# Performance work log

Measured on AMD Instinct MI355X. Metric: run time of the kernel, lower is better.

The kernel has to match this reference:

```python
import jax, jax.numpy as jnp
import numpy as np
from jax import lax

EPS = 1e-6            # cfg.positive
GAUSS_DIM = (32, 32)  # cfg.iou_gauss_dim
TOP_K_CONF = 100      # cfg.nms_top_k_conf
TOP_K_IOU = 20        # cfg.nms_top_k_iou


def unnormal_gaussian(mask_shape, loc):
    # loc: [B, N, 4] = (cx, cy, w, h) in normalized [0,1] coords.
    # Unnormalized anisotropic gaussian rendered on an HxW grid.
    H, W = mask_shape
    cx, cy, w, h = loc[..., 0], loc[..., 1], loc[..., 2], loc[..., 3]
    ys = (jnp.arange(H, dtype=loc.dtype) + 0.5) / H
    xs = (jnp.arange(W, dtype=loc.dtype) + 0.5) / W
    dx = (xs[None, None, None, :] - cx[..., None, None]) / (w[..., None, None] + 1e-4)
    dy = (ys[None, None, :, None] - cy[..., None, None]) / (h[..., None, None] + 1e-4)
    return jnp.exp(-0.5 * (dx * dx + dy * dy))  # [B, N, H, W]


def _take2(t, idx):
    # twoIndexThree: t [B,N,D], idx [B,K] -> [B,K,D]
    return jnp.take_along_axis(t, idx[..., None], axis=1)


def detect(conf, loc, mask):
    # conf: [B,P] object scores; loc: [B,P,4]; mask: [B,P,Dm]
    sorted_conf, idx = lax.top_k(conf, TOP_K_CONF)
    sorted_loc = _take2(loc, idx)
    sorted_mask = _take2(mask, idx)
    g = unnormal_gaussian(GAUSS_DIM, sorted_loc)  # [B,N,Hg,Wg]
    # pairwise gaussian IoU: sum(min) / sum(max); use min+max == a+b identity
    inter = jnp.sum(jnp.minimum(g[:, :, None], g[:, None, :]), axis=(-2, -1))  # [B,N,N]
    s = jnp.sum(g, axis=(-2, -1))
    union = s[:, :, None] + s[:, None, :] - inter
    iou = inter / union
    iou_max = jnp.max(jnp.triu(iou, 1), axis=1)   # max overlap with any earlier (higher-conf) box
    _, keep = lax.top_k(-iou_max, TOP_K_IOU)      # keep K least-overlapping boxes
    return iou, sorted_loc, sorted_mask, sorted_conf, keep


def ae_scaled_loss(original, iou, keep, loc, conf):
    conf_matrix = conf[:, :, None] * conf[:, None, :]   # outer product [B,N,N]
    final_scale = iou * jnp.triu(conf_matrix, 1)
    kept_loc = _take2(loc, keep)                        # [B,K,4]
    # surrogate AutoEncoder per-box loss (AutoEncoder class not in source)
    ae_loss = jnp.mean(kept_loc ** 2, axis=-1)          # [B,K]
    B, N = final_scale.shape[0], final_scale.shape[1]
    K = keep.shape[1]
    ae_grid = jnp.zeros_like(final_scale).at[jnp.arange(B)[:, None], keep].set(
        jnp.broadcast_to(ae_loss[..., None], (B, K, N)))
    return jnp.mean(ae_grid * final_scale)


def variance_loss(original, loc, mask, conf, proto):
    B, C, H, W = original.shape
    Hp, Wp = proto.shape[1], proto.shape[2]
    ug = unnormal_gaussian((Hp, Wp), loc)                           # [B,K,Hp,Wp]
    assembled = jax.nn.sigmoid(jnp.einsum('bhwp,bkp->bkhw', proto, mask))  # lincomb
    attention = assembled * ug
    mc = attention * conf[:, :, None, None]                         # maskConfidence
    denom = jnp.sum(mc, axis=1, keepdims=True) + EPS
    final_conf = 1.0 - jnp.sum(mc * mc / denom, axis=1)             # [B,Hp,Wp]
    final_conf = jnp.where(jnp.isnan(final_conf), 0.0, final_conf)
    # bilinear, align_corners=False == jax linear resize (half-pixel centers)
    resized = jax.image.resize(final_conf[:, None], (B, 1, H, W), method='linear')[:, 0]
    total = jnp.sum(resized, axis=0)                                 # [H,W]
    wmean = jnp.einsum('bchw,bhw->chw', original, resized) / total
    sq = (original - wmean) ** 2
    wvar = sq * resized[:, None] / (total + EPS)
    return jnp.sum(wvar) / Hp * B


def reference(original, loc, conf, mask, proto):
    conf_p = jax.nn.softmax(conf, axis=2)[:, :, 1]
    iou, s_loc, s_mask, s_conf, keep = detect(conf_p, loc, mask)
    ae = ae_scaled_loss(original, iou, keep, s_loc, s_conf)
    k_loc = _take2(s_loc, keep)
    k_mask = _take2(s_mask, keep)
    k_conf = jnp.take_along_axis(s_conf, keep, axis=1)
    var = variance_loss(original, k_loc, k_mask, k_conf, proto)
    return jnp.stack([var, ae])  # [variance_loss, ae_loss]


def setup_inputs() -> dict:
    key = jax.random.key(0)
    k1, k2, k3, k4, k5, k6 = jax.random.split(key, 6)
    B, P, Dm = 2, 19248, 32
    H = W = 550
    Hp = Wp = 138
    original = jax.random.normal(k1, (B, 3, H, W), dtype=jnp.float32)
    centers = jax.random.uniform(k2, (B, P, 2), dtype=jnp.float32)
    sizes = jax.random.uniform(k3, (B, P, 2), dtype=jnp.float32, minval=0.1, maxval=0.5)
    loc = jnp.concatenate([centers, sizes], axis=-1)                 # (cx,cy,w,h)
    conf = jax.random.normal(k4, (B, P, 2), dtype=jnp.float32)
    mask = jax.random.normal(k5, (B, P, Dm), dtype=jnp.float32) * 0.2
    proto = jax.random.normal(k6, (B, Hp, Wp, Dm), dtype=jnp.float32) * 0.5
    return {"original": original, "loc": loc, "conf": conf, "mask": mask, "proto": proto}
```

## Files before the change

kernel.cpp:

```cpp
#include <hip/hip_runtime.h>
#include <hip/hip_bf16.h>
#include <math.h>

constexpr int B   = 2;
constexpr int P   = 19248;
constexpr int N   = 100;
constexpr int K   = 20;
constexpr int GD  = 32;
constexpr int GP  = GD * GD;
constexpr int HP  = 138;
constexpr int HPP = HP * HP;
constexpr int H   = 550;
constexpr int W   = 550;
constexpr int DM  = 32;
constexpr float EPS = 1e-6f;
constexpr int NBIN = 2048;
constexpr int CAND_MAX = 4096;
constexpr int NPAIR = N * (N - 1) / 2;

constexpr int OFS_IDX   = 0;
constexpr int OFS_SCONF = OFS_IDX   + B * N;
constexpr int OFS_SLOC  = OFS_SCONF + B * N;
constexpr int OFS_G     = OFS_SLOC  + B * N * 4;
constexpr int OFS_S     = OFS_G     + B * N * GP;
constexpr int OFS_IOU   = OFS_S     + B * N;
constexpr int OFS_KLOC  = OFS_IOU   + B * N * N;
constexpr int OFS_KMASK = OFS_KLOC  + B * K * 4;
constexpr int OFS_KCONF = OFS_KMASK + B * K * DM;
constexpr int OFS_FC    = OFS_KCONF + B * K;
constexpr int OFS_HIST  = OFS_FC    + B * HPP;
constexpr int OFS_CCNT  = OFS_HIST  + B * NBIN;
constexpr int OFS_T     = OFS_CCNT  + B;
constexpr int OFS_CVAL  = OFS_T     + B;
constexpr int OFS_CIDX  = OFS_CVAL  + B * CAND_MAX;

__device__ __forceinline__ float sig_conf(const float* __restrict__ conf, int b, int p) {
  float c0 = conf[(b * P + p) * 2 + 0];
  float c1 = conf[(b * P + p) * 2 + 1];
  float m  = fmaxf(c0, c1);
  float e0 = expf(c0 - m), e1 = expf(c1 - m);
  return e1 / (e0 + e1);
}

__global__ __launch_bounds__(256) void k_hist(const float* __restrict__ conf,
                                              int* __restrict__ wsi,
                                              float* __restrict__ out) {
  const int b = blockIdx.y, t = threadIdx.x;
  if (blockIdx.x == 0 && b == 0 && t < 2) out[t] = 0.0f;
  __shared__ int sh[NBIN];
  for (int q = t; q < NBIN; q += 256) sh[q] = 0;
  __syncthreads();
  const int base = blockIdx.x * 1024;
#pragma unroll
  for (int q = 0; q < 4; q++) {
    int p = base + q * 256 + t;
    if (p < P) {
      float v = sig_conf(conf, b, p);
      atomicAdd(&sh[__float_as_uint(v) >> 19], 1);
    }
  }
  __syncthreads();
  for (int q = t; q < NBIN; q += 256) {
    int c = sh[q];
    if (c) atomicAdd(&wsi[OFS_HIST + b * NBIN + q], c);
  }
}

__global__ __launch_bounds__(256) void k_thresh(int* __restrict__ wsi) {
  const int b = blockIdx.x, t = threadIdx.x;
  __shared__ int sh[NBIN];
  for (int q = t; q < NBIN; q += 256) sh[q] = wsi[OFS_HIST + b * NBIN + q];
  __syncthreads();
  if (t == 0) {
    int acc = 0, bin = NBIN - 1;
    for (; bin >= 0; bin--) { acc += sh[bin]; if (acc >= N) break; }
    wsi[OFS_T + b] = bin;
  }
}

__global__ __launch_bounds__(256) void k_compact(const float* __restrict__ conf,
                                                 float* __restrict__ wsf,
                                                 int* __restrict__ wsi) {
  const int b = blockIdx.y, t = threadIdx.x;
  const int T = wsi[OFS_T + b];
  const int base = blockIdx.x * 1024;
#pragma unroll
  for (int q = 0; q < 4; q++) {
    int p = base + q * 256 + t;
    if (p < P) {
      float v = sig_conf(conf, b, p);
      if ((int)(__float_as_uint(v) >> 19) >= T) {
        int pos = atomicAdd(&wsi[OFS_CCNT + b], 1);
        if (pos < CAND_MAX) {
          wsf[OFS_CVAL + b * CAND_MAX + pos] = v;
          wsi[OFS_CIDX + b * CAND_MAX + pos] = p;
        }
      }
    }
  }
}

__global__ __launch_bounds__(1024) void k_rank(const float* __restrict__ loc,
                                               float* __restrict__ wsf,
                                               int* __restrict__ wsi) {
  const int b = blockIdx.x, t = threadIdx.x;
  const int M = min(wsi[OFS_CCNT + b], CAND_MAX);
  constexpr int CPT = CAND_MAX / 1024;
  __shared__ float tv[1024];
  __shared__ int   ti[1024];
  __shared__ float outv[N];
  __shared__ int   outi[N];

  float mv[CPT]; int mi[CPT]; int rank[CPT];
#pragma unroll
  for (int q = 0; q < CPT; q++) {
    int c = t + q * 1024;
    rank[q] = 0;
    if (c < M) { mv[q] = wsf[OFS_CVAL + b * CAND_MAX + c]; mi[q] = wsi[OFS_CIDX + b * CAND_MAX + c]; }
    else       { mv[q] = -1.0f; mi[q] = -1; }
  }
  for (int tile = 0; tile < M; tile += 1024) {
    int len = min(1024, M - tile);
    __syncthreads();
    if (t < len) { tv[t] = wsf[OFS_CVAL + b * CAND_MAX + tile + t]; ti[t] = wsi[OFS_CIDX + b * CAND_MAX + tile + t]; }
    __syncthreads();
    for (int j = 0; j < len; j++) {
      float jv = tv[j]; int ji = ti[j];
#pragma unroll
      for (int q = 0; q < CPT; q++)
        rank[q] += (jv > mv[q] || (jv == mv[q] && ji < mi[q])) ? 1 : 0;
    }
  }
#pragma unroll
  for (int q = 0; q < CPT; q++) {
    int c = t + q * 1024;
    if (c < M && rank[q] < N) { outv[rank[q]] = mv[q]; outi[rank[q]] = mi[q]; }
  }
  __syncthreads();

  if (t < N) {
    wsi[OFS_IDX + b * N + t]   = outi[t];
    wsf[OFS_SCONF + b * N + t] = outv[t];
  }
  for (int q = t; q < N * 4; q += 1024) {
    int k = q >> 2, d = q & 3;
    wsf[OFS_SLOC + (b * N + k) * 4 + d] = loc[(b * P + outi[k]) * 4 + d];
  }
}

__global__ __launch_bounds__(256) void ul_gauss_kernel(float* __restrict__ wsf) {
  const int blk = blockIdx.x;
  const int t = threadIdx.x;
  const int i = blk % N;
  const float* l = &wsf[OFS_SLOC + blk * 4];
  const float cx = l[0], cy = l[1], bw = l[2], bh = l[3];
  float* g = &wsf[OFS_G + blk * GP];
  float lsum = 0.0f;
#pragma unroll
  for (int q = 0; q < 4; q++) {
    int pix = t + q * 256;
    int y = pix >> 5, x = pix & 31;
    float dx = ((x + 0.5f) / 32.0f - cx) / (bw + 1e-4f);
    float dy = ((y + 0.5f) / 32.0f - cy) / (bh + 1e-4f);
    float gv = expf(-0.5f * (dx * dx + dy * dy));
    g[pix] = gv;
    lsum += gv;
  }
  for (int q = t; q <= i; q += 256) wsf[OFS_IOU + blk * N + q] = 0.0f;
  for (int off = 32; off > 0; off >>= 1) lsum += __shfl_down(lsum, off);
  __shared__ float sp[4];
  if ((t & 63) == 0) sp[t >> 6] = lsum;
  __syncthreads();
  if (t == 0) wsf[OFS_S + blk] = sp[0] + sp[1] + sp[2] + sp[3];
}

__global__ __launch_bounds__(256) void ul_iou_kernel(float* __restrict__ wsf) {
  const int blk = blockIdx.x;
  const int b = blk / NPAIR;
  const int r = blk - b * NPAIR;
  int i = (int)((199.0f - sqrtf((float)(39601 - 8 * r))) * 0.5f);
  i = min(max(i, 0), N - 2);
  while (i < N - 2 && ((i + 1) * (2 * N - 2 - i)) / 2 <= r) i++;
  while (i > 0 && (i * (2 * N - 1 - i)) / 2 > r) i--;
  const int j = i + 1 + (r - (i * (2 * N - 1 - i)) / 2);

  const int t = threadIdx.x;
  const float* gi = &wsf[OFS_G + (b * N + i) * GP];
  const float* gj = &wsf[OFS_G + (b * N + j) * GP];
  float lsum = 0.0f;
#pragma unroll
  for (int q = 0; q < 4; q++) {
    int pix = t + q * 256;
    lsum += fminf(gi[pix], gj[pix]);
  }
  for (int off = 32; off > 0; off >>= 1) lsum += __shfl_down(lsum, off);
  __shared__ float sp[4];
  if ((t & 63) == 0) sp[t >> 6] = lsum;
  __syncthreads();
  if (t == 0) {
    float inter = sp[0] + sp[1] + sp[2] + sp[3];
    float si = wsf[OFS_S + b * N + i];
    float sj = wsf[OFS_S + b * N + j];
    wsf[OFS_IOU + (b * N + i) * N + j] = inter / (si + sj - inter);
  }
}

__global__ __launch_bounds__(1024) void ul_select_kernel(
    const float* __restrict__ mask, float* __restrict__ wsf,
    int* __restrict__ wsi, float* __restrict__ out) {
  const int b = blockIdx.x;
  const int t = threadIdx.x;
  __shared__ float siou[N * N];
  __shared__ float sconf[N];
  __shared__ unsigned int mbits[N];
  __shared__ int   keep[K];
  __shared__ float coef[K];
  __shared__ float red[16];

  for (int idx = t; idx < N * N; idx += 1024)
    siou[idx] = wsf[OFS_IOU + b * N * N + idx];
  if (t < N) { sconf[t] = wsf[OFS_SCONF + b * N + t]; mbits[t] = 0u; }
  __syncthreads();

  for (int idx = t; idx < N * N; idx += 1024) {
    int col = idx % N;
    atomicMax(&mbits[col], __float_as_uint(siou[idx]));
  }
  __syncthreads();

  if (t < N) {
    unsigned int vb = mbits[t];
    int rank = 0;
    for (int j = 0; j < N; j++) {
      unsigned int jb = mbits[j];
      rank += (jb < vb || (jb == vb && j < t)) ? 1 : 0;
    }
    if (rank < K) keep[rank] = t;
  }
  __syncthreads();

  if (t < K) {
    int r = keep[t];
    float c = sconf[r];
    wsf[OFS_KCONF + b * K + t] = c;
    const float* kl = &wsf[OFS_SLOC + (b * N + r) * 4];
    float ael = 0.25f * (kl[0] * kl[0] + kl[1] * kl[1] + kl[2] * kl[2] + kl[3] * kl[3]);
    coef[t] = ael * c;
  }
  if (t < K * 4) {
    int k = t >> 2, d = t & 3;
    wsf[OFS_KLOC + (b * K + k) * 4 + d] = wsf[OFS_SLOC + (b * N + keep[k]) * 4 + d];
  }
  if (t < K * DM) {
    int k = t >> 5, d = t & 31;
    int orig = wsi[OFS_IDX + b * N + keep[k]];
    wsf[OFS_KMASK + (b * K + k) * DM + d] = mask[(b * P + orig) * DM + d];
  }
  __syncthreads();

  float acc = 0.0f;
  for (int kc = t; kc < K * N; kc += 1024) {
    int k = kc / N, c = kc - k * N;
    int r = keep[k];
    if (c > r) acc += siou[r * N + c] * sconf[c] * coef[k];
  }
  for (int off = 32; off > 0; off >>= 1) acc += __shfl_down(acc, off);
  if ((t & 63) == 0) red[t >> 6] = acc;
  __syncthreads();
  if (t == 0) {
    float s = 0.0f;
    for (int w2 = 0; w2 < 16; w2++) s += red[w2];
    atomicAdd(out + 1, s * (1.0f / (float)(B * N * N)));
  }
}

__global__ __launch_bounds__(256) void ul_fc_kernel(
    const float* __restrict__ proto, float* __restrict__ wsf) {
  const int b = blockIdx.y;
  const int t = threadIdx.x;
  const int pix = blockIdx.x * 256 + t;
  __shared__ float kl[K * 4];
  __shared__ float kc[K];
  __shared__ float km[K * DM];
  for (int q = t; q < K * 4; q += 256) kl[q] = wsf[OFS_KLOC + b * K * 4 + q];
  for (int q = t; q < K; q += 256) kc[q] = wsf[OFS_KCONF + b * K + q];
  for (int q = t; q < K * DM; q += 256) km[q] = wsf[OFS_KMASK + b * K * DM + q];
  __syncthreads();
  if (pix >= HPP) return;
  const int h = pix / HP, w2 = pix - h * HP;

  float pv[DM];
  const float4* pp = (const float4*)&proto[(size_t)(b * HPP + pix) * DM];
#pragma unroll
  for (int q = 0; q < DM / 4; q++) {
    float4 f = pp[q];
    pv[q * 4 + 0] = f.x; pv[q * 4 + 1] = f.y;
    pv[q * 4 + 2] = f.z; pv[q * 4 + 3] = f.w;
  }
  const float ysv = (h + 0.5f) / 138.0f;
  const float xsv = (w2 + 0.5f) / 138.0f;
  float sum1 = 0.0f, sum2 = 0.0f;
#pragma unroll
  for (int k = 0; k < K; k++) {
    float dot = 0.0f;
#pragma unroll
    for (int d = 0; d < DM; d++) dot += pv[d] * km[k * DM + d];
    float a  = 1.0f / (1.0f + expf(-dot));
    float dx = (xsv - kl[k * 4 + 0]) / (kl[k * 4 + 2] + 1e-4f);
    float dy = (ysv - kl[k * 4 + 1]) / (kl[k * 4 + 3] + 1e-4f);
    float ug = expf(-0.5f * (dx * dx + dy * dy));
    float att = a * ug * kc[k];
    sum1 += att;
    sum2 += att * att;
  }
  float fc = 1.0f - sum2 / (sum1 + EPS);
  if (fc != fc) fc = 0.0f;
  wsf[OFS_FC + b * HPP + pix] = fc;
}

__global__ __launch_bounds__(256) void ul_var_kernel(
    const float* __restrict__ orig, const float* __restrict__ wsf,
    float* __restrict__ out) {
  const int t = threadIdx.x;
  const int pix = blockIdx.x * 256 + t;
  float acc = 0.0f;
  if (pix < H * W) {
    const int h = pix / W, w2 = pix - h * W;
    const float sc = 138.0f / 550.0f;
    float sy = (h + 0.5f) * sc - 0.5f;
    float sx = (w2 + 0.5f) * sc - 0.5f;
    float fy0 = floorf(sy), fx0 = floorf(sx);
    float wy = sy - fy0, wx = sx - fx0;
    int y0 = max(0, (int)fy0), y1 = min(HP - 1, (int)fy0 + 1);
    int x0 = max(0, (int)fx0), x1 = min(HP - 1, (int)fx0 + 1);
    float r0, r1;
    {
      const float* fc = &wsf[OFS_FC + 0 * HPP];
      float v00 = fc[y0 * HP + x0], v01 = fc[y0 * HP + x1];
      float v10 = fc[y1 * HP + x0], v11 = fc[y1 * HP + x1];
      float top = v00 + (v01 - v00) * wx;
      float bot = v10 + (v11 - v10) * wx;
      r0 = top + (bot - top) * wy;
    }
    {
      const float* fc = &wsf[OFS_FC + 1 * HPP];
      float v00 = fc[y0 * HP + x0], v01 = fc[y0 * HP + x1];
      float v10 = fc[y1 * HP + x0], v11 = fc[y1 * HP + x1];
      float top = v00 + (v01 - v00) * wx;
      float bot = v10 + (v11 - v10) * wx;
      r1 = top + (bot - top) * wy;
    }
    float total = r0 + r1;
    float inv_t = 1.0f / total;
    float inv_te = 1.0f / (total + EPS);
#pragma unroll
    for (int c = 0; c < 3; c++) {
      float o0 = orig[((0 * 3 + c) * H + h) * W + w2];
      float o1 = orig[((1 * 3 + c) * H + h) * W + w2];
      float wm = (o0 * r0 + o1 * r1) * inv_t;
      float d0 = o0 - wm, d1 = o1 - wm;
      acc += (d0 * d0 * r0 + d1 * d1 * r1) * inv_te;
    }
  }
  for (int off = 32; off > 0; off >>= 1) acc += __shfl_down(acc, off);
  __shared__ float sp[4];
  if ((t & 63) == 0) sp[t >> 6] = acc;
  __syncthreads();
  if (t == 0)
    atomicAdd(out + 0, (sp[0] + sp[1] + sp[2] + sp[3]) * ((float)B / (float)HP));
}

extern "C" void kernel_launch(void* const* d_in, const int* in_sizes, int n_in,
                              void* d_out, int out_size, void* d_ws,
                              size_t ws_size, hipStream_t stream) {
  (void)in_sizes; (void)n_in; (void)out_size; (void)ws_size;
  const float* original = (const float*)d_in[0];
  const float* loc      = (const float*)d_in[1];
  const float* conf     = (const float*)d_in[2];
  const float* mask     = (const float*)d_in[3];
  const float* proto    = (const float*)d_in[4];
  float* out = (float*)d_out;
  float* wsf = (float*)d_ws;
  int*   wsi = (int*)d_ws;

  hipMemsetAsync(wsi + OFS_HIST, 0, (size_t)(B * NBIN + 2 * B) * sizeof(int), stream);

  const int nblk_p = (P + 1023) / 1024;
  k_hist<<<dim3(nblk_p, B), 256, 0, stream>>>(conf, wsi, out);
  k_thresh<<<B, 256, 0, stream>>>(wsi);
  k_compact<<<dim3(nblk_p, B), 256, 0, stream>>>(conf, wsf, wsi);
  k_rank<<<B, 1024, 0, stream>>>(loc, wsf, wsi);
  ul_gauss_kernel<<<B * N, 256, 0, stream>>>(wsf);
  ul_iou_kernel<<<B * NPAIR, 256, 0, stream>>>(wsf);
  ul_select_kernel<<<B, 1024, 0, stream>>>(mask, wsf, wsi, out);
  ul_fc_kernel<<<dim3((HPP + 255) / 256, B), 256, 0, stream>>>(proto, wsf);
  ul_var_kernel<<<(H * W + 255) / 256, 256, 0, stream>>>(original, wsf, out);
}
```

Baseline: 156.1 us.

## Fuse top-k stages into one block, recompute gaussians in IoU, grid-stride variance

Merges the histogram, threshold, compaction and ranking kernels into one kernel per batch that works entirely in shared memory, and drops the memset. The separate gaussian kernel is removed: each IoU pair block recomputes both gaussians and their sums on the fly, so the gaussian buffer is no longer stored or reloaded. The lower-triangle zeroing moves into the select kernel, and the variance kernel becomes a 256-block grid-stride loop. This cuts kernel launches and global traffic, at the cost of doing all top-k work on only two blocks and repeating exp work in every pair block. The candidate buffer is also smaller.

```diff
diff --git a/kernel.cpp b/kernel.cpp
--- a/kernel.cpp
+++ b/kernel.cpp
@@ -15,126 +15,85 @@
 constexpr int DM  = 32;
 constexpr float EPS = 1e-6f;
 constexpr int NBIN = 2048;
-constexpr int CAND_MAX = 4096;
+constexpr int CAND = 2048;
 constexpr int NPAIR = N * (N - 1) / 2;
 
 constexpr int OFS_IDX   = 0;
 constexpr int OFS_SCONF = OFS_IDX   + B * N;
 constexpr int OFS_SLOC  = OFS_SCONF + B * N;
-constexpr int OFS_G     = OFS_SLOC  + B * N * 4;
-constexpr int OFS_S     = OFS_G     + B * N * GP;
-constexpr int OFS_IOU   = OFS_S     + B * N;
+constexpr int OFS_IOU   = OFS_SLOC  + B * N * 4;
 constexpr int OFS_KLOC  = OFS_IOU   + B * N * N;
 constexpr int OFS_KMASK = OFS_KLOC  + B * K * 4;
 constexpr int OFS_KCONF = OFS_KMASK + B * K * DM;
 constexpr int OFS_FC    = OFS_KCONF + B * K;
-constexpr int OFS_HIST  = OFS_FC    + B * HPP;
-constexpr int OFS_CCNT  = OFS_HIST  + B * NBIN;
-constexpr int OFS_T     = OFS_CCNT  + B;
-constexpr int OFS_CVAL  = OFS_T     + B;
-constexpr int OFS_CIDX  = OFS_CVAL  + B * CAND_MAX;
-
-__device__ __forceinline__ float sig_conf(const float* __restrict__ conf, int b, int p) {
-  float c0 = conf[(b * P + p) * 2 + 0];
-  float c1 = conf[(b * P + p) * 2 + 1];
-  float m  = fmaxf(c0, c1);
-  float e0 = expf(c0 - m), e1 = expf(c1 - m);
-  return e1 / (e0 + e1);
-}
-
-__global__ __launch_bounds__(256) void k_hist(const float* __restrict__ conf,
-                                              int* __restrict__ wsi,
-                                              float* __restrict__ out) {
-  const int b = blockIdx.y, t = threadIdx.x;
-  if (blockIdx.x == 0 && b == 0 && t < 2) out[t] = 0.0f;
-  __shared__ int sh[NBIN];
-  for (int q = t; q < NBIN; q += 256) sh[q] = 0;
-  __syncthreads();
-  const int base = blockIdx.x * 1024;
-#pragma unroll
-  for (int q = 0; q < 4; q++) {
-    int p = base + q * 256 + t;
+
+__global__ __launch_bounds__(1024) void k_topk(
+    const float* __restrict__ conf, const float* __restrict__ loc,
+    float* __restrict__ wsf, int* __restrict__ wsi, float* __restrict__ out) {
+  const int b = blockIdx.x;
+  const int t = threadIdx.x;
+  constexpr int EPT = (P + 1023) / 1024;
+  if (b == 0 && t < 2) out[t] = 0.0f;
+
+  __shared__ int   hist[NBIN];
+  __shared__ int   s_T, s_cnt;
+  __shared__ float cv[CAND];
+  __shared__ int   ci[CAND];
+  __shared__ float outv[N];
+  __shared__ int   outi[N];
+
+  for (int q = t; q < NBIN; q += 1024) hist[q] = 0;
+  if (t == 0) s_cnt = 0;
+  __syncthreads();
+
+  float v[EPT];
+#pragma unroll
+  for (int j = 0; j < EPT; j++) {
+    int p = j * 1024 + t;
     if (p < P) {
-      float v = sig_conf(conf, b, p);
-      atomicAdd(&sh[__float_as_uint(v) >> 19], 1);
-    }
-  }
-  __syncthreads();
-  for (int q = t; q < NBIN; q += 256) {
-    int c = sh[q];
-    if (c) atomicAdd(&wsi[OFS_HIST + b * NBIN + q], c);
-  }
-}
-
-__global__ __launch_bounds__(256) void k_thresh(int* __restrict__ wsi) {
-  const int b = blockIdx.x, t = threadIdx.x;
-  __shared__ int sh[NBIN];
-  for (int q = t; q < NBIN; q += 256) sh[q] = wsi[OFS_HIST + b * NBIN + q];
-  __syncthreads();
+      float c0 = conf[(b * P + p) * 2 + 0];
+      float c1 = conf[(b * P + p) * 2 + 1];
+      float m  = fmaxf(c0, c1);
+      float e0 = expf(c0 - m), e1 = expf(c1 - m);
+      v[j] = e1 / (e0 + e1);
+      atomicAdd(&hist[__float_as_uint(v[j]) >> 19], 1);
+    } else {
+      v[j] = -1.0f;
+    }
+  }
+  __syncthreads();
+
   if (t == 0) {
     int acc = 0, bin = NBIN - 1;
-    for (; bin >= 0; bin--) { acc += sh[bin]; if (acc >= N) break; }
-    wsi[OFS_T + b] = bin;
-  }
-}
-
-__global__ __launch_bounds__(256) void k_compact(const float* __restrict__ conf,
-                                                 float* __restrict__ wsf,
-                                                 int* __restrict__ wsi) {
-  const int b = blockIdx.y, t = threadIdx.x;
-  const int T = wsi[OFS_T + b];
-  const int base = blockIdx.x * 1024;
-#pragma unroll
-  for (int q = 0; q < 4; q++) {
-    int p = base + q * 256 + t;
-    if (p < P) {
-      float v = sig_conf(conf, b, p);
-      if ((int)(__float_as_uint(v) >> 19) >= T) {
-        int pos = atomicAdd(&wsi[OFS_CCNT + b], 1);
-        if (pos < CAND_MAX) {
-          wsf[OFS_CVAL + b * CAND_MAX + pos] = v;
-          wsi[OFS_CIDX + b * CAND_MAX + pos] = p;
-        }
+    for (; bin >= 0; bin--) { acc += hist[bin]; if (acc >= N) break; }
+    s_T = bin;
+  }
+  __syncthreads();
+  const int T = s_T;
+
+#pragma unroll
+  for (int j = 0; j < EPT; j++) {
+    int p = j * 1024 + t;
+    if (p < P && (int)(__float_as_uint(v[j]) >> 19) >= T) {
+      int pos = atomicAdd(&s_cnt, 1);
+      if (pos < CAND) { cv[pos] = v[j]; ci[pos] = p; }
+    }
+  }
+  __syncthreads();
+  const int M = min(s_cnt, CAND);
+
+#pragma unroll
+  for (int q = 0; q < CAND / 1024; q++) {
+    int c = t + q * 1024;
+    if (c < M) {
+      float mv = cv[c]; int mi = ci[c];
+      int rank = 0;
+      for (int j = 0; j < M; j++) {
+        float jv = cv[j]; int ji = ci[j];
+        rank += (jv > mv || (jv == mv && ji < mi)) ? 1 : 0;
       }
-    }
-  }
-}
-
-__global__ __launch_bounds__(1024) void k_rank(const float* __restrict__ loc,
-                                               float* __restrict__ wsf,
-                                               int* __restrict__ wsi) {
-  const int b = blockIdx.x, t = threadIdx.x;
-  const int M = min(wsi[OFS_CCNT + b], CAND_MAX);
-  constexpr int CPT = CAND_MAX / 1024;
-  __shared__ float tv[1024];
-  __shared__ int   ti[1024];
-  __shared__ float outv[N];
-  __shared__ int   outi[N];
-
-  float mv[CPT]; int mi[CPT]; int rank[CPT];
-#pragma unroll
-  for (int q = 0; q < CPT; q++) {
-    int c = t + q * 1024;
-    rank[q] = 0;
-    if (c < M) { mv[q] = wsf[OFS_CVAL + b * CAND_MAX + c]; mi[q] = wsi[OFS_CIDX + b * CAND_MAX + c]; }
-    else       { mv[q] = -1.0f; mi[q] = -1; }
-  }
-  for (int tile = 0; tile < M; tile += 1024) {
-    int len = min(1024, M - tile);
-    __syncthreads();
-    if (t < len) { tv[t] = wsf[OFS_CVAL + b * CAND_MAX + tile + t]; ti[t] = wsi[OFS_CIDX + b * CAND_MAX + tile + t]; }
-    __syncthreads();
-    for (int j = 0; j < len; j++) {
-      float jv = tv[j]; int ji = ti[j];
-#pragma unroll
-      for (int q = 0; q < CPT; q++)
-        rank[q] += (jv > mv[q] || (jv == mv[q] && ji < mi[q])) ? 1 : 0;
-    }
-  }
-#pragma unroll
-  for (int q = 0; q < CPT; q++) {
-    int c = t + q * 1024;
-    if (c < M && rank[q] < N) { outv[rank[q]] = mv[q]; outi[rank[q]] = mi[q]; }
+      if (rank < N) { outv[rank] = mv; outi[rank] = mi; }
+    }
   }
   __syncthreads();
 
@@ -142,39 +101,13 @@
     wsi[OFS_IDX + b * N + t]   = outi[t];
     wsf[OFS_SCONF + b * N + t] = outv[t];
   }
-  for (int q = t; q < N * 4; q += 1024) {
-    int k = q >> 2, d = q & 3;
+  if (t < N * 4) {
+    int k = t >> 2, d = t & 3;
     wsf[OFS_SLOC + (b * N + k) * 4 + d] = loc[(b * P + outi[k]) * 4 + d];
   }
 }
 
-__global__ __launch_bounds__(256) void ul_gauss_kernel(float* __restrict__ wsf) {
-  const int blk = blockIdx.x;
-  const int t = threadIdx.x;
-  const int i = blk % N;
-  const float* l = &wsf[OFS_SLOC + blk * 4];
-  const float cx = l[0], cy = l[1], bw = l[2], bh = l[3];
-  float* g = &wsf[OFS_G + blk * GP];
-  float lsum = 0.0f;
-#pragma unroll
-  for (int q = 0; q < 4; q++) {
-    int pix = t + q * 256;
-    int y = pix >> 5, x = pix & 31;
-    float dx = ((x + 0.5f) / 32.0f - cx) / (bw + 1e-4f);
-    float dy = ((y + 0.5f) / 32.0f - cy) / (bh + 1e-4f);
-    float gv = expf(-0.5f * (dx * dx + dy * dy));
-    g[pix] = gv;
-    lsum += gv;
-  }
-  for (int q = t; q <= i; q += 256) wsf[OFS_IOU + blk * N + q] = 0.0f;
-  for (int off = 32; off > 0; off >>= 1) lsum += __shfl_down(lsum, off);
-  __shared__ float sp[4];
-  if ((t & 63) == 0) sp[t >> 6] = lsum;
-  __syncthreads();
-  if (t == 0) wsf[OFS_S + blk] = sp[0] + sp[1] + sp[2] + sp[3];
-}
-
-__global__ __launch_bounds__(256) void ul_iou_kernel(float* __restrict__ wsf) {
+__global__ __launch_bounds__(256) void k_iou(float* __restrict__ wsf) {
   const int blk = blockIdx.x;
   const int b = blk / NPAIR;
   const int r = blk - b * NPAIR;
@@ -185,27 +118,47 @@
   const int j = i + 1 + (r - (i * (2 * N - 1 - i)) / 2);
 
   const int t = threadIdx.x;
-  const float* gi = &wsf[OFS_G + (b * N + i) * GP];
-  const float* gj = &wsf[OFS_G + (b * N + j) * GP];
-  float lsum = 0.0f;
+  const float* li = &wsf[OFS_SLOC + (b * N + i) * 4];
+  const float* lj = &wsf[OFS_SLOC + (b * N + j) * 4];
+  const float cxi = li[0], cyi = li[1], wi = li[2], hi = li[3];
+  const float cxj = lj[0], cyj = lj[1], wj = lj[2], hj = lj[3];
+
+  float smin = 0.0f, ssi = 0.0f, ssj = 0.0f;
 #pragma unroll
   for (int q = 0; q < 4; q++) {
     int pix = t + q * 256;
-    lsum += fminf(gi[pix], gj[pix]);
-  }
-  for (int off = 32; off > 0; off >>= 1) lsum += __shfl_down(lsum, off);
-  __shared__ float sp[4];
-  if ((t & 63) == 0) sp[t >> 6] = lsum;
+    int y = pix >> 5, x = pix & 31;
+    float xs = (x + 0.5f) / 32.0f, ys = (y + 0.5f) / 32.0f;
+    float dxi = (xs - cxi) / (wi + 1e-4f);
+    float dyi = (ys - cyi) / (hi + 1e-4f);
+    float gi = expf(-0.5f * (dxi * dxi + dyi * dyi));
+    float dxj = (xs - cxj) / (wj + 1e-4f);
+    float dyj = (ys - cyj) / (hj + 1e-4f);
+    float gj = expf(-0.5f * (dxj * dxj + dyj * dyj));
+    smin += fminf(gi, gj);
+    ssi += gi;
+    ssj += gj;
+  }
+  for (int off = 32; off > 0; off >>= 1) {
+    smin += __shfl_down(smin, off);
+    ssi  += __shfl_down(ssi, off);
+    ssj  += __shfl_down(ssj, off);
+  }
+  __shared__ float sp[3][4];
+  if ((t & 63) == 0) {
+    int w4 = t >> 6;
+    sp[0][w4] = smin; sp[1][w4] = ssi; sp[2][w4] = ssj;
+  }
   __syncthreads();
   if (t == 0) {
-    float inter = sp[0] + sp[1] + sp[2] + sp[3];
-    float si = wsf[OFS_S + b * N + i];
-    float sj = wsf[OFS_S + b * N + j];
+    float inter = sp[0][0] + sp[0][1] + sp[0][2] + sp[0][3];
+    float si    = sp[1][0] + sp[1][1] + sp[1][2] + sp[1][3];
+    float sj    = sp[2][0] + sp[2][1] + sp[2][2] + sp[2][3];
     wsf[OFS_IOU + (b * N + i) * N + j] = inter / (si + sj - inter);
   }
 }
 
-__global__ __launch_bounds__(1024) void ul_select_kernel(
+__global__ __launch_bounds__(1024) void k_select(
     const float* __restrict__ mask, float* __restrict__ wsf,
     int* __restrict__ wsi, float* __restrict__ out) {
   const int b = blockIdx.x;
@@ -217,8 +170,10 @@
   __shared__ float coef[K];
   __shared__ float red[16];
 
-  for (int idx = t; idx < N * N; idx += 1024)
-    siou[idx] = wsf[OFS_IOU + b * N * N + idx];
+  for (int idx = t; idx < N * N; idx += 1024) {
+    int row = idx / N, col = idx - row * N;
+    siou[idx] = (col > row) ? wsf[OFS_IOU + b * N * N + idx] : 0.0f;
+  }
   if (t < N) { sconf[t] = wsf[OFS_SCONF + b * N + t]; mbits[t] = 0u; }
   __syncthreads();
 
@@ -274,7 +229,7 @@
   }
 }
 
-__global__ __launch_bounds__(256) void ul_fc_kernel(
+__global__ __launch_bounds__(256) void k_fc(
     const float* __restrict__ proto, float* __restrict__ wsf) {
   const int b = blockIdx.y;
   const int t = threadIdx.x;
@@ -318,13 +273,12 @@
   wsf[OFS_FC + b * HPP + pix] = fc;
 }
 
-__global__ __launch_bounds__(256) void ul_var_kernel(
+__global__ __launch_bounds__(256) void k_var(
     const float* __restrict__ orig, const float* __restrict__ wsf,
     float* __restrict__ out) {
   const int t = threadIdx.x;
-  const int pix = blockIdx.x * 256 + t;
   float acc = 0.0f;
-  if (pix < H * W) {
+  for (int pix = blockIdx.x * 256 + t; pix < H * W; pix += 256 * 256) {
     const int h = pix / W, w2 = pix - h * W;
     const float sc = 138.0f / 550.0f;
     float sy = (h + 0.5f) * sc - 0.5f;
@@ -383,16 +337,9 @@
   float* wsf = (float*)d_ws;
   int*   wsi = (int*)d_ws;
 
-  hipMemsetAsync(wsi + OFS_HIST, 0, (size_t)(B * NBIN + 2 * B) * sizeof(int), stream);
-
-  const int nblk_p = (P + 1023) / 1024;
-  k_hist<<<dim3(nblk_p, B), 256, 0, stream>>>(conf, wsi, out);
-  k_thresh<<<B, 256, 0, stream>>>(wsi);
-  k_compact<<<dim3(nblk_p, B), 256, 0, stream>>>(conf, wsf, wsi);
-  k_rank<<<B, 1024, 0, stream>>>(loc, wsf, wsi);
-  ul_gauss_kernel<<<B * N, 256, 0, stream>>>(wsf);
-  ul_iou_kernel<<<B * NPAIR, 256, 0, stream>>>(wsf);
-  ul_select_kernel<<<B, 1024, 0, stream>>>(mask, wsf, wsi, out);
-  ul_fc_kernel<<<dim3((HPP + 255) / 256, B), 256, 0, stream>>>(proto, wsf);
-  ul_var_kernel<<<(H * W + 255) / 256, 256, 0, stream>>>(original, wsf, out);
-}
+  k_topk<<<B, 1024, 0, stream>>>(conf, loc, wsf, wsi, out);
+  k_iou<<<B * NPAIR, 256, 0, stream>>>(wsf);
+  k_select<<<B, 1024, 0, stream>>>(mask, wsf, wsi, out);
+  k_fc<<<dim3((HPP + 255) / 256, B), 256, 0, stream>>>(proto, wsf);
+  k_var<<<256, 256, 0, stream>>>(original, wsf, out);
+}
```

New measurement: 134.6 us. -13.8%, faster.
